# Optimization experiments

Hardware: AMD Instinct MI355X
Metric: run time of the kernel (lower is better)

Reference implementation:

```python
import jax, jax.numpy as jnp
import numpy as np

T, B, D_IN, HID, D_OUT = 512, 64, 1024, 512, 10


def _gru_dir(x, w_ih, w_hh, b_ih, b_hh, reverse):
    # x: [T,B,D]; w_ih: [3H,D]; w_hh: [3H,H]; biases: [3H]
    xp = jnp.einsum('tbd,gd->tbg', x, w_ih) + b_ih  # [T,B,3H]
    if reverse:
        xp = xp[::-1]
    H = w_hh.shape[1]

    def step(h, xt):
        gh = h @ w_hh.T + b_hh                      # [B,3H]
        xr, xz, xn = jnp.split(xt, 3, axis=-1)
        hr, hz, hn = jnp.split(gh, 3, axis=-1)
        r = jax.nn.sigmoid(xr + hr)
        z = jax.nn.sigmoid(xz + hz)
        n = jnp.tanh(xn + r * hn)
        h_new = (1.0 - z) * n + z * h
        return h_new, h_new

    h0 = jnp.zeros((x.shape[1], H), x.dtype)
    _, hs = jax.lax.scan(step, h0, xp)              # [T,B,H]
    if reverse:
        hs = hs[::-1]
    return hs


def setup_inputs() -> dict:
    key = jax.random.key(0)
    ks = jax.random.split(key, 20)
    k = 1.0 / np.sqrt(HID)
    u = lambda kk, sh, lim: jax.random.uniform(kk, sh, jnp.float32, -lim, lim)
    inp = {
        'numerical': jax.random.normal(ks[0], (B, 8), jnp.float32),
        'embedding': jax.random.normal(ks[1], (T, B, D_IN), jnp.float32),
        # GRU forward direction
        'w_ih_f': u(ks[2], (3 * HID, D_IN), k),
        'w_hh_f': u(ks[3], (3 * HID, HID), k),
        'b_ih_f': u(ks[4], (3 * HID,), k),
        'b_hh_f': u(ks[5], (3 * HID,), k),
        # GRU backward direction
        'w_ih_b': u(ks[6], (3 * HID, D_IN), k),
        'w_hh_b': u(ks[7], (3 * HID, HID), k),
        'b_ih_b': u(ks[8], (3 * HID,), k),
        'b_hh_b': u(ks[9], (3 * HID,), k),
        # attention params (normal std 0.05 per _create_weights)
        'attn_w': 0.05 * jax.random.normal(ks[10], (2 * HID, 2 * HID), jnp.float32),
        'attn_b': 0.05 * jax.random.normal(ks[11], (1, 2 * HID), jnp.float32),
        'ctx_w': 0.05 * jax.random.normal(ks[12], (2 * HID, 1), jnp.float32),
        # classifier: Linear(D_in -> hidden) -> ReLU -> Linear(hidden -> D_out)
        'cls_w1': u(ks[13], (D_IN, HID), 1.0 / np.sqrt(D_IN)),
        'cls_b1': u(ks[14], (HID,), 1.0 / np.sqrt(D_IN)),
        'cls_w2': u(ks[15], (HID, D_OUT), 1.0 / np.sqrt(HID)),
        'cls_b2': u(ks[16], (D_OUT,), 1.0 / np.sqrt(HID)),
    }
    return inp


def reference(numerical, embedding,
              w_ih_f, w_hh_f, b_ih_f, b_hh_f,
              w_ih_b, w_hh_b, b_ih_b, b_hh_b,
              attn_w, attn_b, ctx_w,
              cls_w1, cls_b1, cls_w2, cls_b2):
    # bidirectional GRU: [T,B,2H]
    hf = _gru_dir(embedding, w_ih_f, w_hh_f, b_ih_f, b_hh_f, reverse=False)
    hb = _gru_dir(embedding, w_ih_b, w_hh_b, b_ih_b, b_hh_b, reverse=True)
    f_output = jnp.concatenate([hf, hb], axis=-1)
    # additive attention: tanh(f W + b), then tanh(. @ ctx) -> scores [T,B]
    att = jnp.tanh(jnp.einsum('tbd,de->tbe', f_output, attn_w) + attn_b)
    scores = jnp.tanh(att @ ctx_w)[..., 0]          # [T,B]
    w = jax.nn.softmax(scores.T, axis=1)            # [B,T]
    ctx = jnp.einsum('tbd,bt->bd', f_output, w)     # [B,2H]
    # classifier
    hid = jax.nn.relu(ctx @ cls_w1 + cls_b1)
    out = hid @ cls_w2 + cls_b2                     # [B,D_OUT]
    return out
```

## Files before the change

### kernel.cpp

```cpp
#include <hip/hip_runtime.h>
#include <stdint.h>

#define T_   512
#define B_   64
#define DIN  1024
#define HID  512
#define G3   1536
#define NC   3072
#define MROWS 32768

typedef __bf16 bf16;
typedef __bf16 bf16x8 __attribute__((ext_vector_type(8)));
typedef float  f32x4  __attribute__((ext_vector_type(4)));

#define GLOBAL_AS __attribute__((address_space(1)))
#define LDS_AS    __attribute__((address_space(3)))

__device__ __forceinline__ uint16_t f2bf_bits(float x){
  union{float f; uint32_t u;} v; v.f = x;
  uint32_t u = v.u;
  u += 0x7FFFu + ((u >> 16) & 1u);
  return (uint16_t)(u >> 16);
}
__device__ __forceinline__ float bf2f_bits(uint16_t h){
  union{uint32_t u; float f;} v; v.u = ((uint32_t)h) << 16;
  return v.f;
}
__device__ __forceinline__ float sig_f(float x){
  return 1.f/(1.f + __expf(-x));
}
__device__ __forceinline__ float tanh_f(float x){
  return 1.f - 2.f/(1.f + __expf(2.f*x));
}

__global__ void k_conv_emb(const float* __restrict__ src, uint16_t* __restrict__ dst, long n8){
  long i = (long)blockIdx.x*blockDim.x + threadIdx.x;
  if(i >= n8) return;
  const float4* s = (const float4*)src;
  float4 a = s[i*2], b = s[i*2+1];
  uint32_t p0 = (uint32_t)f2bf_bits(a.x) | ((uint32_t)f2bf_bits(a.y) << 16);
  uint32_t p1 = (uint32_t)f2bf_bits(a.z) | ((uint32_t)f2bf_bits(a.w) << 16);
  uint32_t p2 = (uint32_t)f2bf_bits(b.x) | ((uint32_t)f2bf_bits(b.y) << 16);
  uint32_t p3 = (uint32_t)f2bf_bits(b.z) | ((uint32_t)f2bf_bits(b.w) << 16);
  ((uint4*)dst)[i] = make_uint4(p0,p1,p2,p3);
}

__global__ void k_conv_wcat(const float* __restrict__ wf, const float* __restrict__ wb, uint16_t* __restrict__ dst, int n){
  int i = blockIdx.x*256 + threadIdx.x;
  if(i >= n) return;
  float v = (i < G3*DIN) ? wf[i] : wb[i - G3*DIN];
  dst[i] = f2bf_bits(v);
}

__global__ void k_conv_awt(const float* __restrict__ aw, uint16_t* __restrict__ dst, int n){
  int i = blockIdx.x*256 + threadIdx.x;
  if(i >= n) return;
  int e = i >> 10, d = i & 1023;
  dst[i] = f2bf_bits(aw[d*1024 + e]);
}

__global__ void k_conv_whh(const float* __restrict__ wf, const float* __restrict__ wb, uint4* __restrict__ wmem){
  int idx = blockIdx.x*256 + threadIdx.x;
  if(idx >= 2*16*96*64) return;
  int c  = idx & 63;
  int t2 = idx >> 6;
  int lc = t2 % 96;
  int t3 = t2 / 96;
  int member = t3 & 15, dir = t3 >> 4;
  int ct = lc >> 4, rr = lc & 15;
  int gcol = (ct >> 1)*512 + member*32 + (ct & 1)*16 + rr;
  int csrc = c ^ (lc & 7);
  const float* src = (dir ? wb : wf) + (size_t)gcol*512 + csrc*8;
  float4 f0 = *(const float4*)src;
  float4 f1 = *(const float4*)(src + 4);
  uint32_t p0 = (uint32_t)f2bf_bits(f0.x) | ((uint32_t)f2bf_bits(f0.y) << 16);
  uint32_t p1 = (uint32_t)f2bf_bits(f0.z) | ((uint32_t)f2bf_bits(f0.w) << 16);
  uint32_t p2 = (uint32_t)f2bf_bits(f1.x) | ((uint32_t)f2bf_bits(f1.y) << 16);
  uint32_t p3 = (uint32_t)f2bf_bits(f1.z) | ((uint32_t)f2bf_bits(f1.w) << 16);
  wmem[idx] = make_uint4(p0,p1,p2,p3);
}

__launch_bounds__(256)
__global__ void k_gemm_xp(const uint16_t* __restrict__ A, const uint16_t* __restrict__ Bw,
                          const float* __restrict__ bihf, const float* __restrict__ bihb,
                          uint16_t* __restrict__ C)
{
  __shared__ uint16_t lA[2][128*32];
  __shared__ uint16_t lB[2][128*32];
  const int K = 1024;
  int bn = blockIdx.x, bm = blockIdx.y;
  int tid = threadIdx.x;
  int lane = tid & 63, wid = tid >> 6;
  int wm = wid >> 1, wn = wid & 1;
  int rowBase = bm*128, colBase = bn*128;
  int rg = lane >> 4, rr = lane & 15;

  auto stage = [&](int buf, int kt){
    #pragma unroll
    for(int i=0;i<2;i++){
      int e = (i*256 + tid)*8;
      int r = e >> 5, c = e & 31;
      __builtin_amdgcn_global_load_lds((const GLOBAL_AS void*)(A + (size_t)(rowBase + r)*K + kt*32 + c),
                                       (LDS_AS void*)&lA[buf][e], 16, 0, 0);
    }
    #pragma unroll
    for(int i=0;i<2;i++){
      int e = (i*256 + tid)*8;
      int r = e >> 5, c = e & 31;
      __builtin_amdgcn_global_load_lds((const GLOBAL_AS void*)(Bw + (size_t)(colBase + r)*K + kt*32 + c),
                                       (LDS_AS void*)&lB[buf][e], 16, 0, 0);
    }
  };

  f32x4 acc[4][4];
  #pragma unroll
  for(int mi=0;mi<4;mi++)
    #pragma unroll
    for(int ni=0;ni<4;ni++) acc[mi][ni] = (f32x4){0.f,0.f,0.f,0.f};

  stage(0, 0);
  __syncthreads();
  for(int kt=0; kt<32; kt++){
    int buf = kt & 1;
    if(kt+1 < 32) stage(buf^1, kt+1);
    bf16x8 af[4], bfv[4];
    #pragma unroll
    for(int mi=0;mi<4;mi++)
      af[mi] = *(const bf16x8*)&lA[buf][(wm*64 + mi*16 + rr)*32 + rg*8];
    #pragma unroll
    for(int ni=0;ni<4;ni++)
      bfv[ni] = *(const bf16x8*)&lB[buf][(wn*64 + ni*16 + rr)*32 + rg*8];
    #pragma unroll
    for(int mi=0;mi<4;mi++)
      #pragma unroll
      for(int ni=0;ni<4;ni++)
        acc[mi][ni] = __builtin_amdgcn_mfma_f32_16x16x32_bf16(af[mi], bfv[ni], acc[mi][ni], 0,0,0);
    __syncthreads();
  }

  #pragma unroll
  for(int ni=0;ni<4;ni++){
    int col = colBase + wn*64 + ni*16 + rr;
    float bv = (col < G3) ? bihf[col] : bihb[col - G3];
    int dircol = (col >= G3) ? 1 : 0;
    int cm = col - dircol*G3;
    int g  = cm >> 9;
    int j  = cm & 511;
    int mem = j >> 5, cc = j & 31;
    #pragma unroll
    for(int mi=0;mi<4;mi++){
      int row0 = rowBase + wm*64 + mi*16 + rg*4;
      int tt = row0 >> 6;
      int b0 = row0 & 63;
      int bgx = b0 >> 4, rr0 = b0 & 15;
      size_t ob = (((((size_t)dircol*512 + tt)*4 + bgx)*16 + mem)*3 + g)*512 + rr0*32 + cc;
      C[ob]      = f2bf_bits(acc[mi][ni][0]+bv);
      C[ob+32]   = f2bf_bits(acc[mi][ni][1]+bv);
      C[ob+64]   = f2bf_bits(acc[mi][ni][2]+bv);
      C[ob+96]   = f2bf_bits(acc[mi][ni][3]+bv);
    }
  }
}

__launch_bounds__(256)
__global__ void k_gemm_att(const uint16_t* __restrict__ A, const uint16_t* __restrict__ Bw,
                           const float* __restrict__ attn_b, const float* __restrict__ ctx_w,
                           float* __restrict__ scores_raw)
{
  __shared__ uint16_t lA[2][128*32];
  __shared__ uint16_t lB[2][128*32];
  const int K = 1024;
  int bn = blockIdx.x, bm = blockIdx.y;
  int tid = threadIdx.x;
  int lane = tid & 63, wid = tid >> 6;
  int wm = wid >> 1, wn = wid & 1;
  int rowBase = bm*128, colBase = bn*128;
  int rg = lane >> 4, rr = lane & 15;

  auto stage = [&](int buf, int kt){
    #pragma unroll
    for(int i=0;i<2;i++){
      int e = (i*256 + tid)*8;
      int r = e >> 5, c = e & 31;
      __builtin_amdgcn_global_load_lds((const GLOBAL_AS void*)(A + (size_t)(rowBase + r)*K + kt*32 + c),
                                       (LDS_AS void*)&lA[buf][e], 16, 0, 0);
    }
    #pragma unroll
    for(int i=0;i<2;i++){
      int e = (i*256 + tid)*8;
      int r = e >> 5, c = e & 31;
      __builtin_amdgcn_global_load_lds((const GLOBAL_AS void*)(Bw + (size_t)(colBase + r)*K + kt*32 + c),
                                       (LDS_AS void*)&lB[buf][e], 16, 0, 0);
    }
  };

  f32x4 acc[4][4];
  #pragma unroll
  for(int mi=0;mi<4;mi++)
    #pragma unroll
    for(int ni=0;ni<4;ni++) acc[mi][ni] = (f32x4){0.f,0.f,0.f,0.f};

  stage(0, 0);
  __syncthreads();
  for(int kt=0; kt<32; kt++){
    int buf = kt & 1;
    if(kt+1 < 32) stage(buf^1, kt+1);
    bf16x8 af[4], bfv[4];
    #pragma unroll
    for(int mi=0;mi<4;mi++)
      af[mi] = *(const bf16x8*)&lA[buf][(wm*64 + mi*16 + rr)*32 + rg*8];
    #pragma unroll
    for(int ni=0;ni<4;ni++)
      bfv[ni] = *(const bf16x8*)&lB[buf][(wn*64 + ni*16 + rr)*32 + rg*8];
    #pragma unroll
    for(int mi=0;mi<4;mi++)
      #pragma unroll
      for(int ni=0;ni<4;ni++)
        acc[mi][ni] = __builtin_amdgcn_mfma_f32_16x16x32_bf16(af[mi], bfv[ni], acc[mi][ni], 0,0,0);
    __syncthreads();
  }

  float ab[4], cw[4];
  #pragma unroll
  for(int ni=0;ni<4;ni++){
    int col = colBase + wn*64 + ni*16 + rr;
    ab[ni] = attn_b[col];
    cw[ni] = ctx_w[col];
  }
  #pragma unroll
  for(int mi=0;mi<4;mi++){
    #pragma unroll
    for(int r=0;r<4;r++){
      float part = 0.f;
      #pragma unroll
      for(int ni=0;ni<4;ni++) part += tanhf(acc[mi][ni][r] + ab[ni]) * cw[ni];
      #pragma unroll
      for(int off=1; off<16; off<<=1) part += __shfl_xor(part, off);
      if(rr == 0){
        int row = rowBase + wm*64 + mi*16 + rg*4 + r;
        atomicAdd(&scores_raw[row], part);
      }
    }
  }
}

__launch_bounds__(768, 3)
__global__ void k_recur(const uint16_t* __restrict__ xp,
                        const uint4* __restrict__ wmem,
                        const float* __restrict__ bhhf, const float* __restrict__ bhhb,
                        unsigned long long* __restrict__ tagbuf,
                        uint16_t* __restrict__ f_out)
{
  __shared__ uint16_t Wl[96*512];
  __shared__ uint16_t hl[16*512];
  __shared__ float    ghl[2*6*16*17];

  int bid = blockIdx.x;
  int dir = bid & 1, bg = (bid >> 1) & 3, member = bid >> 3;
  int jb = member*32;
  int tid = threadIdx.x;
  int lane = tid & 63, w = tid >> 6;
  int rr = lane & 15, rg = lane >> 4;
  int ct = w >> 1, kh = w & 1;

  const uint4* wsrc = wmem + (size_t)(dir*16 + member)*6144;
  for(int e = tid; e < 6144; e += 768)
    __builtin_amdgcn_global_load_lds((const GLOBAL_AS void*)(wsrc + e),
                                     (LDS_AS void*)&Wl[e*8], 16, 0, 0);
  for(int i = tid; i < 2*6*16*17; i += 768) ghl[i] = 0.f;

  int gcol = tid & 31;
  const float* bhh = dir ? bhhb : bhhf;
  float bR = 0.f, bZ = 0.f, bN = 0.f, hprev = 0.f;
  if(tid < 512){
    bR = bhh[jb + gcol];
    bZ = bhh[512 + jb + gcol];
    bN = bhh[1024 + jb + gcol];
  }

  int srow = tid >> 5;
  int sbase = tid & 31;
  int cswz = ((sbase >> 2) ^ (srow & 7));
  int lpos0 = srow*512 + cswz*8 + (sbase & 3)*2;

  __syncthreads();

  #pragma unroll 1
  for(int t = 0; t < 512; t++){
    int trow = dir ? (511 - t) : t;

    uint16_t xr16 = 0, xz16 = 0, xn16 = 0;
    if(tid < 512){
      const uint16_t* xb = xp + (((((size_t)dir*512 + trow)*4 + bg)*16 + member)*3)*512;
      xr16 = xb[tid];
      xz16 = xb[512 + tid];
      xn16 = xb[1024 + tid];
    }

    if(t > 0 && tid < 512){
      const unsigned long long* tb =
        tagbuf + ((size_t)((dir*2 + ((t-1) & 1))*4 + bg)*16 + srow)*256 + sbase;
      unsigned want = (unsigned)t;
      unsigned long long v0,v1,v2,v3,v4,v5,v6,v7;
      v0 = __hip_atomic_load(tb +   0, __ATOMIC_RELAXED, __HIP_MEMORY_SCOPE_AGENT);
      v1 = __hip_atomic_load(tb +  32, __ATOMIC_RELAXED, __HIP_MEMORY_SCOPE_AGENT);
      v2 = __hip_atomic_load(tb +  64, __ATOMIC_RELAXED, __HIP_MEMORY_SCOPE_AGENT);
      v3 = __hip_atomic_load(tb +  96, __ATOMIC_RELAXED, __HIP_MEMORY_SCOPE_AGENT);
      v4 = __hip_atomic_load(tb + 128, __ATOMIC_RELAXED, __HIP_MEMORY_SCOPE_AGENT);
      v5 = __hip_atomic_load(tb + 160, __ATOMIC_RELAXED, __HIP_MEMORY_SCOPE_AGENT);
      v6 = __hip_atomic_load(tb + 192, __ATOMIC_RELAXED, __HIP_MEMORY_SCOPE_AGENT);
      v7 = __hip_atomic_load(tb + 224, __ATOMIC_RELAXED, __HIP_MEMORY_SCOPE_AGENT);
      bool o0 = ((unsigned)v0 == want), o1 = ((unsigned)v1 == want);
      bool o2 = ((unsigned)v2 == want), o3 = ((unsigned)v3 == want);
      bool o4 = ((unsigned)v4 == want), o5 = ((unsigned)v5 == want);
      bool o6 = ((unsigned)v6 == want), o7 = ((unsigned)v7 == want);
      while(!(o0 & o1 & o2 & o3 & o4 & o5 & o6 & o7)){
        if(!o0){ v0 = __hip_atomic_load(tb +   0, __ATOMIC_RELAXED, __HIP_MEMORY_SCOPE_AGENT); o0 = ((unsigned)v0 == want); }
        if(!o1){ v1 = __hip_atomic_load(tb +  32, __ATOMIC_RELAXED, __HIP_MEMORY_SCOPE_AGENT); o1 = ((unsigned)v1 == want); }
        if(!o2){ v2 = __hip_atomic_load(tb +  64, __ATOMIC_RELAXED, __HIP_MEMORY_SCOPE_AGENT); o2 = ((unsigned)v2 == want); }
        if(!o3){ v3 = __hip_atomic_load(tb +  96, __ATOMIC_RELAXED, __HIP_MEMORY_SCOPE_AGENT); o3 = ((unsigned)v3 == want); }
        if(!o4){ v4 = __hip_atomic_load(tb + 128, __ATOMIC_RELAXED, __HIP_MEMORY_SCOPE_AGENT); o4 = ((unsigned)v4 == want); }
        if(!o5){ v5 = __hip_atomic_load(tb + 160, __ATOMIC_RELAXED, __HIP_MEMORY_SCOPE_AGENT); o5 = ((unsigned)v5 == want); }
        if(!o6){ v6 = __hip_atomic_load(tb + 192, __ATOMIC_RELAXED, __HIP_MEMORY_SCOPE_AGENT); o6 = ((unsigned)v6 == want); }
        if(!o7){ v7 = __hip_atomic_load(tb + 224, __ATOMIC_RELAXED, __HIP_MEMORY_SCOPE_AGENT); o7 = ((unsigned)v7 == want); }
      }
      *(uint32_t*)&hl[lpos0 +   0] = (uint32_t)(v0 >> 32);
      *(uint32_t*)&hl[lpos0 +  64] = (uint32_t)(v1 >> 32);
      *(uint32_t*)&hl[lpos0 + 128] = (uint32_t)(v2 >> 32);
      *(uint32_t*)&hl[lpos0 + 192] = (uint32_t)(v3 >> 32);
      *(uint32_t*)&hl[lpos0 + 256] = (uint32_t)(v4 >> 32);
      *(uint32_t*)&hl[lpos0 + 320] = (uint32_t)(v5 >> 32);
      *(uint32_t*)&hl[lpos0 + 384] = (uint32_t)(v6 >> 32);
      *(uint32_t*)&hl[lpos0 + 448] = (uint32_t)(v7 >> 32);
    }
    __syncthreads();

    if(t > 0){
      f32x4 acc = (f32x4){0.f,0.f,0.f,0.f};
      #pragma unroll
      for(int ks = 0; ks < 8; ks++){
        int ch = kh*32 + ks*4 + rg;
        int sw = (ch ^ (rr & 7))*8;
        bf16x8 a = *(const bf16x8*)&hl[rr*512 + sw];
        bf16x8 b = *(const bf16x8*)&Wl[(ct*16 + rr)*512 + sw];
        acc = __builtin_amdgcn_mfma_f32_16x16x32_bf16(a, b, acc, 0,0,0);
      }
      #pragma unroll
      for(int j = 0; j < 4; j++)
        ghl[((kh*6 + ct)*16 + rg*4 + j)*17 + rr] = acc[j];
    }
    __syncthreads();

    if(tid < 512){
      int grow = tid >> 5;
      int c16 = gcol >> 4, cc = gcol & 15;
      float gR = ghl[((0 + c16)*16 + grow)*17 + cc] + ghl[((6  + c16)*16 + grow)*17 + cc] + bR;
      float gZ = ghl[((2 + c16)*16 + grow)*17 + cc] + ghl[((8  + c16)*16 + grow)*17 + cc] + bZ;
      float gN = ghl[((4 + c16)*16 + grow)*17 + cc] + ghl[((10 + c16)*16 + grow)*17 + cc] + bN;
      float rv = sig_f(bf2f_bits(xr16) + gR);
      float zv = sig_f(bf2f_bits(xz16) + gZ);
      float nv = tanh_f(bf2f_bits(xn16) + rv*gN);
      float hnew = (1.f - zv)*nv + zv*hprev;
      hprev = hnew;
      unsigned hb = (unsigned)f2bf_bits(hnew);
      unsigned nb = (unsigned)__shfl_down((int)hb, 1);
      if((tid & 1) == 0){
        unsigned pk = hb | (nb << 16);
        int slot = member*16 + (gcol >> 1);
        unsigned long long pv = ((unsigned long long)pk << 32) | (unsigned)(t + 1);
        __hip_atomic_store(
          tagbuf + ((size_t)((dir*2 + (t & 1))*4 + bg)*16 + grow)*256 + slot,
          pv, __ATOMIC_RELAXED, __HIP_MEMORY_SCOPE_AGENT);
        *(unsigned*)&f_out[((size_t)trow*64 + bg*16 + grow)*1024 + dir*512 + jb + gcol] = pk;
      }
    }
  }
}

__global__ void k_softmax(const float* __restrict__ scores_raw, float* __restrict__ wsm){
  __shared__ float sv[512];
  __shared__ float red[8];
  int b = blockIdx.x;
  int tid = threadIdx.x;
  float mymax = -1e30f;
  for(int t = tid; t < 512; t += 256){
    float s = tanhf(scores_raw[t*64 + b]);
    sv[t] = s;
    mymax = fmaxf(mymax, s);
  }
  #pragma unroll
  for(int off=1; off<64; off<<=1) mymax = fmaxf(mymax, __shfl_xor(mymax, off));
  if((tid&63)==0) red[tid>>6] = mymax;
  __syncthreads();
  float bmax = fmaxf(fmaxf(red[0],red[1]), fmaxf(red[2],red[3]));
  __syncthreads();
  float mysum = 0.f;
  for(int t = tid; t < 512; t += 256){
    float e = __expf(sv[t] - bmax);
    sv[t] = e;
    mysum += e;
  }
  #pragma unroll
  for(int off=1; off<64; off<<=1) mysum += __shfl_xor(mysum, off);
  if((tid&63)==0) red[tid>>6] = mysum;
  __syncthreads();
  float inv = 1.f/(red[0]+red[1]+red[2]+red[3]);
  for(int t = tid; t < 512; t += 256) wsm[b*512 + t] = sv[t]*inv;
}

__global__ void k_ctx(const uint16_t* __restrict__ f_out, const float* __restrict__ wsm, float* __restrict__ ctx){
  __shared__ float wloc[512];
  int b = blockIdx.x >> 2, chunk = blockIdx.x & 3;
  int tid = threadIdx.x;
  for(int t = tid; t < 512; t += 256) wloc[t] = wsm[b*512 + t];
  __syncthreads();
  int d = chunk*256 + tid;
  float acc = 0.f;
  #pragma unroll 8
  for(int t = 0; t < 512; t++)
    acc += wloc[t] * bf2f_bits(f_out[(size_t)(t*64 + b)*1024 + d]);
  ctx[b*1024 + d] = acc;
}

__global__ void k_cls1(const float* __restrict__ ctx, const float* __restrict__ w1,
                       const float* __restrict__ b1, float* __restrict__ hid){
  int idx = blockIdx.x*256 + threadIdx.x;
  int b = idx >> 9, h = idx & 511;
  float acc = b1[h];
  for(int d = 0; d < 1024; d++) acc += ctx[b*1024 + d] * w1[d*512 + h];
  hid[idx] = fmaxf(acc, 0.f);
}

__global__ void k_cls2(const float* __restrict__ hid, const float* __restrict__ w2,
                       const float* __restrict__ b2, float* __restrict__ out){
  int idx = threadIdx.x;
  if(idx >= 640) return;
  int b = idx / 10, o = idx % 10;
  float acc = b2[o];
  for(int h = 0; h < 512; h++) acc += hid[b*512 + h] * w2[h*10 + o];
  out[idx] = acc;
}

extern "C" void kernel_launch(void* const* d_in, const int* in_sizes, int n_in,
                              void* d_out, int out_size, void* d_ws, size_t ws_size,
                              hipStream_t stream)
{
  const float* emb    = (const float*)d_in[1];
  const float* w_ih_f = (const float*)d_in[2];
  const float* w_hh_f = (const float*)d_in[3];
  const float* b_ih_f = (const float*)d_in[4];
  const float* b_hh_f = (const float*)d_in[5];
  const float* w_ih_b = (const float*)d_in[6];
  const float* w_hh_b = (const float*)d_in[7];
  const float* b_ih_b = (const float*)d_in[8];
  const float* b_hh_b = (const float*)d_in[9];
  const float* attn_w = (const float*)d_in[10];
  const float* attn_b = (const float*)d_in[11];
  const float* ctx_w  = (const float*)d_in[12];
  const float* cls_w1 = (const float*)d_in[13];
  const float* cls_b1 = (const float*)d_in[14];
  const float* cls_w2 = (const float*)d_in[15];
  const float* cls_b2 = (const float*)d_in[16];
  float* out = (float*)d_out;

  char* ws = (char*)d_ws;
  size_t off = 0;
  auto alloc = [&](size_t bytes){ void* p = ws + off; off += (bytes + 255) & ~(size_t)255; return p; };
  uint16_t* femb = (uint16_t*)alloc((size_t)MROWS*DIN*2);
  uint16_t* wcat = (uint16_t*)alloc((size_t)NC*DIN*2);
  uint16_t* xp   = (uint16_t*)alloc((size_t)MROWS*NC*2);
  uint16_t* awT  = (uint16_t*)alloc((size_t)1024*1024*2);
  uint4*    wmem = (uint4*)alloc((size_t)2*16*96*64*16);
  unsigned long long* tagbuf = (unsigned long long*)alloc((size_t)2*2*4*16*256*8);
  float* scraw   = (float*)alloc((size_t)MROWS*4);
  float* wsm     = (float*)alloc((size_t)B_*T_*4);
  float* ctx     = (float*)alloc((size_t)B_*1024*4);
  float* hid     = (float*)alloc((size_t)B_*512*4);

  hipMemsetAsync(tagbuf, 0, (size_t)2*2*4*16*256*8, stream);
  hipMemsetAsync(scraw, 0, (size_t)MROWS*4, stream);

  k_conv_emb<<<16384, 256, 0, stream>>>(emb, femb, (long)MROWS*DIN/8);
  k_conv_wcat<<<12288, 256, 0, stream>>>(w_ih_f, w_ih_b, wcat, NC*DIN);
  k_conv_awt<<<4096, 256, 0, stream>>>(attn_w, awT, 1024*1024);
  k_conv_whh<<<768, 256, 0, stream>>>(w_hh_f, w_hh_b, wmem);

  k_gemm_xp<<<dim3(24,256), 256, 0, stream>>>(femb, wcat, b_ih_f, b_ih_b, xp);

  k_recur<<<128, 768, 0, stream>>>(xp, wmem, b_hh_f, b_hh_b, tagbuf, femb );

  k_gemm_att<<<dim3(8,256), 256, 0, stream>>>(femb, awT, attn_b, ctx_w, scraw);
  k_softmax<<<64, 256, 0, stream>>>(scraw, wsm);
  k_ctx<<<256, 256, 0, stream>>>(femb, wsm, ctx);
  k_cls1<<<128, 256, 0, stream>>>(ctx, cls_w1, cls_b1, hid);
  k_cls2<<<1, 640, 0, stream>>>(hid, cls_w2, cls_b2, out);
}
```

Measured before the change: 1.720 ms.

## Interleave forward and backward GRU directions per block with register-resident weights

The recurrent kernel now runs both directions in one block (64 blocks instead of 128) and alternates forward and backward half-steps. Each direction's tag polling and x-projection loads are issued early, so one direction's cross-block wait overlaps the other's compute. Recurrent weights move from LDS into VGPRs held by empty asm constraints, which frees the LDS tile and removes the per-step LDS weight reads. In exchange, per-block serial work doubles and register pressure rises under the 768-thread launch bound, which may force spills.

Result: slower. 2.430 ms (+41.3%).

```diff
diff --git a/kernel.cpp b/kernel.cpp
--- a/kernel.cpp
+++ b/kernel.cpp
@@ -16,6 +16,8 @@
 #define GLOBAL_AS __attribute__((address_space(1)))
 #define LDS_AS    __attribute__((address_space(3)))
 
+#define LDT(p) __hip_atomic_load((p), __ATOMIC_RELAXED, __HIP_MEMORY_SCOPE_AGENT)
+
 __device__ __forceinline__ uint16_t f2bf_bits(float x){
   union{float f; uint32_t u;} v; v.f = x;
   uint32_t u = v.u;
@@ -31,6 +33,9 @@
 }
 __device__ __forceinline__ float tanh_f(float x){
   return 1.f - 2.f/(1.f + __expf(2.f*x));
+}
+__device__ __forceinline__ bf16x8 as_bf16x8(uint4 u){
+  union{uint4 a; bf16x8 b;} c; c.a = u; return c.b;
 }
 
 __global__ void k_conv_emb(const float* __restrict__ src, uint16_t* __restrict__ dst, long n8){
@@ -251,117 +256,144 @@
                         unsigned long long* __restrict__ tagbuf,
                         uint16_t* __restrict__ f_out)
 {
-  __shared__ uint16_t Wl[96*512];
   __shared__ uint16_t hl[16*512];
   __shared__ float    ghl[2*6*16*17];
 
   int bid = blockIdx.x;
-  int dir = bid & 1, bg = (bid >> 1) & 3, member = bid >> 3;
+  int bg = bid & 3, member = bid >> 2;
   int jb = member*32;
   int tid = threadIdx.x;
   int lane = tid & 63, w = tid >> 6;
   int rr = lane & 15, rg = lane >> 4;
   int ct = w >> 1, kh = w & 1;
-
-  const uint4* wsrc = wmem + (size_t)(dir*16 + member)*6144;
-  for(int e = tid; e < 6144; e += 768)
-    __builtin_amdgcn_global_load_lds((const GLOBAL_AS void*)(wsrc + e),
-                                     (LDS_AS void*)&Wl[e*8], 16, 0, 0);
+  int xm = rr & 7;
+
+  const uint4* wsl0 = wmem + (size_t)member*6144 + (ct*16 + rr)*64;
+  const uint4* wsl1 = wmem + (size_t)(16 + member)*6144 + (ct*16 + rr)*64;
+  uint4 wa0 = wsl0[(kh*32 +  0 + rg) ^ xm];
+  uint4 wa1 = wsl0[(kh*32 +  4 + rg) ^ xm];
+  uint4 wa2 = wsl0[(kh*32 +  8 + rg) ^ xm];
+  uint4 wa3 = wsl0[(kh*32 + 12 + rg) ^ xm];
+  uint4 wa4 = wsl0[(kh*32 + 16 + rg) ^ xm];
+  uint4 wa5 = wsl0[(kh*32 + 20 + rg) ^ xm];
+  uint4 wa6 = wsl0[(kh*32 + 24 + rg) ^ xm];
+  uint4 wa7 = wsl0[(kh*32 + 28 + rg) ^ xm];
+  uint4 wb0 = wsl1[(kh*32 +  0 + rg) ^ xm];
+  uint4 wb1 = wsl1[(kh*32 +  4 + rg) ^ xm];
+  uint4 wb2 = wsl1[(kh*32 +  8 + rg) ^ xm];
+  uint4 wb3 = wsl1[(kh*32 + 12 + rg) ^ xm];
+  uint4 wb4 = wsl1[(kh*32 + 16 + rg) ^ xm];
+  uint4 wb5 = wsl1[(kh*32 + 20 + rg) ^ xm];
+  uint4 wb6 = wsl1[(kh*32 + 24 + rg) ^ xm];
+  uint4 wb7 = wsl1[(kh*32 + 28 + rg) ^ xm];
+  asm volatile("" :: "v"(wa0.x), "v"(wa0.y), "v"(wa0.z), "v"(wa0.w),
+                     "v"(wa1.x), "v"(wa1.y), "v"(wa1.z), "v"(wa1.w));
+  asm volatile("" :: "v"(wa2.x), "v"(wa2.y), "v"(wa2.z), "v"(wa2.w),
+                     "v"(wa3.x), "v"(wa3.y), "v"(wa3.z), "v"(wa3.w));
+  asm volatile("" :: "v"(wa4.x), "v"(wa4.y), "v"(wa4.z), "v"(wa4.w),
+                     "v"(wa5.x), "v"(wa5.y), "v"(wa5.z), "v"(wa5.w));
+  asm volatile("" :: "v"(wa6.x), "v"(wa6.y), "v"(wa6.z), "v"(wa6.w),
+                     "v"(wa7.x), "v"(wa7.y), "v"(wa7.z), "v"(wa7.w));
+  asm volatile("" :: "v"(wb0.x), "v"(wb0.y), "v"(wb0.z), "v"(wb0.w),
+                     "v"(wb1.x), "v"(wb1.y), "v"(wb1.z), "v"(wb1.w));
+  asm volatile("" :: "v"(wb2.x), "v"(wb2.y), "v"(wb2.z), "v"(wb2.w),
+                     "v"(wb3.x), "v"(wb3.y), "v"(wb3.z), "v"(wb3.w));
+  asm volatile("" :: "v"(wb4.x), "v"(wb4.y), "v"(wb4.z), "v"(wb4.w),
+                     "v"(wb5.x), "v"(wb5.y), "v"(wb5.z), "v"(wb5.w));
+  asm volatile("" :: "v"(wb6.x), "v"(wb6.y), "v"(wb6.z), "v"(wb6.w),
+                     "v"(wb7.x), "v"(wb7.y), "v"(wb7.z), "v"(wb7.w));
+
   for(int i = tid; i < 2*6*16*17; i += 768) ghl[i] = 0.f;
 
   int gcol = tid & 31;
-  const float* bhh = dir ? bhhb : bhhf;
-  float bR = 0.f, bZ = 0.f, bN = 0.f, hprev = 0.f;
+  float bR0=0,bZ0=0,bN0=0,bR1=0,bZ1=0,bN1=0, hA=0.f, hB=0.f;
   if(tid < 512){
-    bR = bhh[jb + gcol];
-    bZ = bhh[512 + jb + gcol];
-    bN = bhh[1024 + jb + gcol];
-  }
-
-  int srow = tid >> 5;
-  int sbase = tid & 31;
-  int cswz = ((sbase >> 2) ^ (srow & 7));
+    bR0 = bhhf[jb + gcol]; bZ0 = bhhf[512 + jb + gcol]; bN0 = bhhf[1024 + jb + gcol];
+    bR1 = bhhb[jb + gcol]; bZ1 = bhhb[512 + jb + gcol]; bN1 = bhhb[1024 + jb + gcol];
+  }
+
+  int srow = tid >> 5, sbase = tid & 31;
+  int cswz = (sbase >> 2) ^ (srow & 7);
   int lpos0 = srow*512 + cswz*8 + (sbase & 3)*2;
 
+  unsigned long long pA0=0,pA1=0,pA2=0,pA3=0,pA4=0,pA5=0,pA6=0,pA7=0;
+  unsigned long long pB0=0,pB1=0,pB2=0,pB3=0,pB4=0,pB5=0,pB6=0,pB7=0;
+  uint16_t xAr=0,xAz=0,xAn=0, xBr=0,xBz=0,xBn=0;
+
+  if(tid < 512){
+    const uint16_t* xb = xp + (((size_t)bg*16 + member)*3)*512;
+    xAr = xb[tid]; xAz = xb[512 + tid]; xAn = xb[1024 + tid];
+  }
   __syncthreads();
 
   #pragma unroll 1
   for(int t = 0; t < 512; t++){
-    int trow = dir ? (511 - t) : t;
-
-    uint16_t xr16 = 0, xz16 = 0, xn16 = 0;
-    if(tid < 512){
-      const uint16_t* xb = xp + (((((size_t)dir*512 + trow)*4 + bg)*16 + member)*3)*512;
-      xr16 = xb[tid];
-      xz16 = xb[512 + tid];
-      xn16 = xb[1024 + tid];
-    }
-
     if(t > 0 && tid < 512){
       const unsigned long long* tb =
-        tagbuf + ((size_t)((dir*2 + ((t-1) & 1))*4 + bg)*16 + srow)*256 + sbase;
+        tagbuf + ((size_t)(((t-1)&1)*4 + bg)*16 + srow)*256 + sbase;
       unsigned want = (unsigned)t;
-      unsigned long long v0,v1,v2,v3,v4,v5,v6,v7;
-      v0 = __hip_atomic_load(tb +   0, __ATOMIC_RELAXED, __HIP_MEMORY_SCOPE_AGENT);
-      v1 = __hip_atomic_load(tb +  32, __ATOMIC_RELAXED, __HIP_MEMORY_SCOPE_AGENT);
-      v2 = __hip_atomic_load(tb +  64, __ATOMIC_RELAXED, __HIP_MEMORY_SCOPE_AGENT);
-      v3 = __hip_atomic_load(tb +  96, __ATOMIC_RELAXED, __HIP_MEMORY_SCOPE_AGENT);
-      v4 = __hip_atomic_load(tb + 128, __ATOMIC_RELAXED, __HIP_MEMORY_SCOPE_AGENT);
-      v5 = __hip_atomic_load(tb + 160, __ATOMIC_RELAXED, __HIP_MEMORY_SCOPE_AGENT);
-      v6 = __hip_atomic_load(tb + 192, __ATOMIC_RELAXED, __HIP_MEMORY_SCOPE_AGENT);
-      v7 = __hip_atomic_load(tb + 224, __ATOMIC_RELAXED, __HIP_MEMORY_SCOPE_AGENT);
-      bool o0 = ((unsigned)v0 == want), o1 = ((unsigned)v1 == want);
-      bool o2 = ((unsigned)v2 == want), o3 = ((unsigned)v3 == want);
-      bool o4 = ((unsigned)v4 == want), o5 = ((unsigned)v5 == want);
-      bool o6 = ((unsigned)v6 == want), o7 = ((unsigned)v7 == want);
-      while(!(o0 & o1 & o2 & o3 & o4 & o5 & o6 & o7)){
-        if(!o0){ v0 = __hip_atomic_load(tb +   0, __ATOMIC_RELAXED, __HIP_MEMORY_SCOPE_AGENT); o0 = ((unsigned)v0 == want); }
-        if(!o1){ v1 = __hip_atomic_load(tb +  32, __ATOMIC_RELAXED, __HIP_MEMORY_SCOPE_AGENT); o1 = ((unsigned)v1 == want); }
-        if(!o2){ v2 = __hip_atomic_load(tb +  64, __ATOMIC_RELAXED, __HIP_MEMORY_SCOPE_AGENT); o2 = ((unsigned)v2 == want); }
-        if(!o3){ v3 = __hip_atomic_load(tb +  96, __ATOMIC_RELAXED, __HIP_MEMORY_SCOPE_AGENT); o3 = ((unsigned)v3 == want); }
-        if(!o4){ v4 = __hip_atomic_load(tb + 128, __ATOMIC_RELAXED, __HIP_MEMORY_SCOPE_AGENT); o4 = ((unsigned)v4 == want); }
-        if(!o5){ v5 = __hip_atomic_load(tb + 160, __ATOMIC_RELAXED, __HIP_MEMORY_SCOPE_AGENT); o5 = ((unsigned)v5 == want); }
-        if(!o6){ v6 = __hip_atomic_load(tb + 192, __ATOMIC_RELAXED, __HIP_MEMORY_SCOPE_AGENT); o6 = ((unsigned)v6 == want); }
-        if(!o7){ v7 = __hip_atomic_load(tb + 224, __ATOMIC_RELAXED, __HIP_MEMORY_SCOPE_AGENT); o7 = ((unsigned)v7 == want); }
+      bool ok = ((unsigned)pA0==want)&((unsigned)pA1==want)&((unsigned)pA2==want)&((unsigned)pA3==want)
+              & ((unsigned)pA4==want)&((unsigned)pA5==want)&((unsigned)pA6==want)&((unsigned)pA7==want);
+      while(!ok){
+        pA0 = LDT(tb+0);   pA1 = LDT(tb+32);  pA2 = LDT(tb+64);  pA3 = LDT(tb+96);
+        pA4 = LDT(tb+128); pA5 = LDT(tb+160); pA6 = LDT(tb+192); pA7 = LDT(tb+224);
+        ok = ((unsigned)pA0==want)&((unsigned)pA1==want)&((unsigned)pA2==want)&((unsigned)pA3==want)
+           & ((unsigned)pA4==want)&((unsigned)pA5==want)&((unsigned)pA6==want)&((unsigned)pA7==want);
       }
-      *(uint32_t*)&hl[lpos0 +   0] = (uint32_t)(v0 >> 32);
-      *(uint32_t*)&hl[lpos0 +  64] = (uint32_t)(v1 >> 32);
-      *(uint32_t*)&hl[lpos0 + 128] = (uint32_t)(v2 >> 32);
-      *(uint32_t*)&hl[lpos0 + 192] = (uint32_t)(v3 >> 32);
-      *(uint32_t*)&hl[lpos0 + 256] = (uint32_t)(v4 >> 32);
-      *(uint32_t*)&hl[lpos0 + 320] = (uint32_t)(v5 >> 32);
-      *(uint32_t*)&hl[lpos0 + 384] = (uint32_t)(v6 >> 32);
-      *(uint32_t*)&hl[lpos0 + 448] = (uint32_t)(v7 >> 32);
+      *(uint32_t*)&hl[lpos0 +   0] = (uint32_t)(pA0 >> 32);
+      *(uint32_t*)&hl[lpos0 +  64] = (uint32_t)(pA1 >> 32);
+      *(uint32_t*)&hl[lpos0 + 128] = (uint32_t)(pA2 >> 32);
+      *(uint32_t*)&hl[lpos0 + 192] = (uint32_t)(pA3 >> 32);
+      *(uint32_t*)&hl[lpos0 + 256] = (uint32_t)(pA4 >> 32);
+      *(uint32_t*)&hl[lpos0 + 320] = (uint32_t)(pA5 >> 32);
+      *(uint32_t*)&hl[lpos0 + 384] = (uint32_t)(pA6 >> 32);
+      *(uint32_t*)&hl[lpos0 + 448] = (uint32_t)(pA7 >> 32);
+    }
+    if(tid < 512){
+      if(t > 0){
+        const unsigned long long* tb =
+          tagbuf + ((size_t)((2 + ((t-1)&1))*4 + bg)*16 + srow)*256 + sbase;
+        pB0 = LDT(tb+0);   pB1 = LDT(tb+32);  pB2 = LDT(tb+64);  pB3 = LDT(tb+96);
+        pB4 = LDT(tb+128); pB5 = LDT(tb+160); pB6 = LDT(tb+192); pB7 = LDT(tb+224);
+      }
+      const uint16_t* xb = xp + (((((size_t)512 + (511 - t))*4 + bg)*16 + member)*3)*512;
+      xBr = xb[tid]; xBz = xb[512 + tid]; xBn = xb[1024 + tid];
     }
     __syncthreads();
-
     if(t > 0){
       f32x4 acc = (f32x4){0.f,0.f,0.f,0.f};
-      #pragma unroll
-      for(int ks = 0; ks < 8; ks++){
-        int ch = kh*32 + ks*4 + rg;
-        int sw = (ch ^ (rr & 7))*8;
-        bf16x8 a = *(const bf16x8*)&hl[rr*512 + sw];
-        bf16x8 b = *(const bf16x8*)&Wl[(ct*16 + rr)*512 + sw];
-        acc = __builtin_amdgcn_mfma_f32_16x16x32_bf16(a, b, acc, 0,0,0);
-      }
+      bf16x8 a0 = *(const bf16x8*)&hl[rr*512 + ((kh*32 +  0 + rg) ^ xm)*8];
+      acc = __builtin_amdgcn_mfma_f32_16x16x32_bf16(a0, as_bf16x8(wa0), acc, 0,0,0);
+      bf16x8 a1 = *(const bf16x8*)&hl[rr*512 + ((kh*32 +  4 + rg) ^ xm)*8];
+      acc = __builtin_amdgcn_mfma_f32_16x16x32_bf16(a1, as_bf16x8(wa1), acc, 0,0,0);
+      bf16x8 a2 = *(const bf16x8*)&hl[rr*512 + ((kh*32 +  8 + rg) ^ xm)*8];
+      acc = __builtin_amdgcn_mfma_f32_16x16x32_bf16(a2, as_bf16x8(wa2), acc, 0,0,0);
+      bf16x8 a3 = *(const bf16x8*)&hl[rr*512 + ((kh*32 + 12 + rg) ^ xm)*8];
+      acc = __builtin_amdgcn_mfma_f32_16x16x32_bf16(a3, as_bf16x8(wa3), acc, 0,0,0);
+      bf16x8 a4 = *(const bf16x8*)&hl[rr*512 + ((kh*32 + 16 + rg) ^ xm)*8];
+      acc = __builtin_amdgcn_mfma_f32_16x16x32_bf16(a4, as_bf16x8(wa4), acc, 0,0,0);
+      bf16x8 a5 = *(const bf16x8*)&hl[rr*512 + ((kh*32 + 20 + rg) ^ xm)*8];
+      acc = __builtin_amdgcn_mfma_f32_16x16x32_bf16(a5, as_bf16x8(wa5), acc, 0,0,0);
+      bf16x8 a6 = *(const bf16x8*)&hl[rr*512 + ((kh*32 + 24 + rg) ^ xm)*8];
+      acc = __builtin_amdgcn_mfma_f32_16x16x32_bf16(a6, as_bf16x8(wa6), acc, 0,0,0);
+      bf16x8 a7 = *(const bf16x8*)&hl[rr*512 + ((kh*32 + 28 + rg) ^ xm)*8];
+      acc = __builtin_amdgcn_mfma_f32_16x16x32_bf16(a7, as_bf16x8(wa7), acc, 0,0,0);
       #pragma unroll
       for(int j = 0; j < 4; j++)
         ghl[((kh*6 + ct)*16 + rg*4 + j)*17 + rr] = acc[j];
     }
     __syncthreads();
-
     if(tid < 512){
       int grow = tid >> 5;
       int c16 = gcol >> 4, cc = gcol & 15;
-      float gR = ghl[((0 + c16)*16 + grow)*17 + cc] + ghl[((6  + c16)*16 + grow)*17 + cc] + bR;
-      float gZ = ghl[((2 + c16)*16 + grow)*17 + cc] + ghl[((8  + c16)*16 + grow)*17 + cc] + bZ;
-      float gN = ghl[((4 + c16)*16 + grow)*17 + cc] + ghl[((10 + c16)*16 + grow)*17 + cc] + bN;
-      float rv = sig_f(bf2f_bits(xr16) + gR);
-      float zv = sig_f(bf2f_bits(xz16) + gZ);
-      float nv = tanh_f(bf2f_bits(xn16) + rv*gN);
-      float hnew = (1.f - zv)*nv + zv*hprev;
-      hprev = hnew;
+      float gR = ghl[((0 + c16)*16 + grow)*17 + cc] + ghl[((6  + c16)*16 + grow)*17 + cc] + bR0;
+      float gZ = ghl[((2 + c16)*16 + grow)*17 + cc] + ghl[((8  + c16)*16 + grow)*17 + cc] + bZ0;
+      float gN = ghl[((4 + c16)*16 + grow)*17 + cc] + ghl[((10 + c16)*16 + grow)*17 + cc] + bN0;
+      float rv = sig_f(bf2f_bits(xAr) + gR);
+      float zv = sig_f(bf2f_bits(xAz) + gZ);
+      float nv = tanh_f(bf2f_bits(xAn) + rv*gN);
+      float hnew = (1.f - zv)*nv + zv*hA;
+      hA = hnew;
       unsigned hb = (unsigned)f2bf_bits(hnew);
       unsigned nb = (unsigned)__shfl_down((int)hb, 1);
       if((tid & 1) == 0){
@@ -369,9 +401,86 @@
         int slot = member*16 + (gcol >> 1);
         unsigned long long pv = ((unsigned long long)pk << 32) | (unsigned)(t + 1);
         __hip_atomic_store(
-          tagbuf + ((size_t)((dir*2 + (t & 1))*4 + bg)*16 + grow)*256 + slot,
+          tagbuf + ((size_t)((t&1)*4 + bg)*16 + grow)*256 + slot,
           pv, __ATOMIC_RELAXED, __HIP_MEMORY_SCOPE_AGENT);
-        *(unsigned*)&f_out[((size_t)trow*64 + bg*16 + grow)*1024 + dir*512 + jb + gcol] = pk;
+        *(unsigned*)&f_out[((size_t)t*64 + bg*16 + grow)*1024 + jb + gcol] = pk;
+      }
+    }
+
+    if(t > 0 && tid < 512){
+      const unsigned long long* tb =
+        tagbuf + ((size_t)((2 + ((t-1)&1))*4 + bg)*16 + srow)*256 + sbase;
+      unsigned want = (unsigned)t;
+      bool ok = ((unsigned)pB0==want)&((unsigned)pB1==want)&((unsigned)pB2==want)&((unsigned)pB3==want)
+              & ((unsigned)pB4==want)&((unsigned)pB5==want)&((unsigned)pB6==want)&((unsigned)pB7==want);
+      while(!ok){
+        pB0 = LDT(tb+0);   pB1 = LDT(tb+32);  pB2 = LDT(tb+64);  pB3 = LDT(tb+96);
+        pB4 = LDT(tb+128); pB5 = LDT(tb+160); pB6 = LDT(tb+192); pB7 = LDT(tb+224);
+        ok = ((unsigned)pB0==want)&((unsigned)pB1==want)&((unsigned)pB2==want)&((unsigned)pB3==want)
+           & ((unsigned)pB4==want)&((unsigned)pB5==want)&((unsigned)pB6==want)&((unsigned)pB7==want);
+      }
+      *(uint32_t*)&hl[lpos0 +   0] = (uint32_t)(pB0 >> 32);
+      *(uint32_t*)&hl[lpos0 +  64] = (uint32_t)(pB1 >> 32);
+      *(uint32_t*)&hl[lpos0 + 128] = (uint32_t)(pB2 >> 32);
+      *(uint32_t*)&hl[lpos0 + 192] = (uint32_t)(pB3 >> 32);
+      *(uint32_t*)&hl[lpos0 + 256] = (uint32_t)(pB4 >> 32);
+      *(uint32_t*)&hl[lpos0 + 320] = (uint32_t)(pB5 >> 32);
+      *(uint32_t*)&hl[lpos0 + 384] = (uint32_t)(pB6 >> 32);
+      *(uint32_t*)&hl[lpos0 + 448] = (uint32_t)(pB7 >> 32);
+    }
+    if(tid < 512){
+      const unsigned long long* tb =
+        tagbuf + ((size_t)((t&1)*4 + bg)*16 + srow)*256 + sbase;
+      pA0 = LDT(tb+0);   pA1 = LDT(tb+32);  pA2 = LDT(tb+64);  pA3 = LDT(tb+96);
+      pA4 = LDT(tb+128); pA5 = LDT(tb+160); pA6 = LDT(tb+192); pA7 = LDT(tb+224);
+      const uint16_t* xb = xp + (((((size_t)(t + 1))*4 + bg)*16 + member)*3)*512;
+      xAr = xb[tid]; xAz = xb[512 + tid]; xAn = xb[1024 + tid];
+    }
+    __syncthreads();
+    if(t > 0){
+      f32x4 acc = (f32x4){0.f,0.f,0.f,0.f};
+      bf16x8 a0 = *(const bf16x8*)&hl[rr*512 + ((kh*32 +  0 + rg) ^ xm)*8];
+      acc = __builtin_amdgcn_mfma_f32_16x16x32_bf16(a0, as_bf16x8(wb0), acc, 0,0,0);
+      bf16x8 a1 = *(const bf16x8*)&hl[rr*512 + ((kh*32 +  4 + rg) ^ xm)*8];
+      acc = __builtin_amdgcn_mfma_f32_16x16x32_bf16(a1, as_bf16x8(wb1), acc, 0,0,0);
+      bf16x8 a2 = *(const bf16x8*)&hl[rr*512 + ((kh*32 +  8 + rg) ^ xm)*8];
+      acc = __builtin_amdgcn_mfma_f32_16x16x32_bf16(a2, as_bf16x8(wb2), acc, 0,0,0);
+      bf16x8 a3 = *(const bf16x8*)&hl[rr*512 + ((kh*32 + 12 + rg) ^ xm)*8];
+      acc = __builtin_amdgcn_mfma_f32_16x16x32_bf16(a3, as_bf16x8(wb3), acc, 0,0,0);
+      bf16x8 a4 = *(const bf16x8*)&hl[rr*512 + ((kh*32 + 16 + rg) ^ xm)*8];
+      acc = __builtin_amdgcn_mfma_f32_16x16x32_bf16(a4, as_bf16x8(wb4), acc, 0,0,0);
+      bf16x8 a5 = *(const bf16x8*)&hl[rr*512 + ((kh*32 + 20 + rg) ^ xm)*8];
+      acc = __builtin_amdgcn_mfma_f32_16x16x32_bf16(a5, as_bf16x8(wb5), acc, 0,0,0);
+      bf16x8 a6 = *(const bf16x8*)&hl[rr*512 + ((kh*32 + 24 + rg) ^ xm)*8];
+      acc = __builtin_amdgcn_mfma_f32_16x16x32_bf16(a6, as_bf16x8(wb6), acc, 0,0,0);
+      bf16x8 a7 = *(const bf16x8*)&hl[rr*512 + ((kh*32 + 28 + rg) ^ xm)*8];
+      acc = __builtin_amdgcn_mfma_f32_16x16x32_bf16(a7, as_bf16x8(wb7), acc, 0,0,0);
+      #pragma unroll
+      for(int j = 0; j < 4; j++)
+        ghl[((kh*6 + ct)*16 + rg*4 + j)*17 + rr] = acc[j];
+    }
+    __syncthreads();
+    if(tid < 512){
+      int grow = tid >> 5;
+      int c16 = gcol >> 4, cc = gcol & 15;
+      float gR = ghl[((0 + c16)*16 + grow)*17 + cc] + ghl[((6  + c16)*16 + grow)*17 + cc] + bR1;
+      float gZ = ghl[((2 + c16)*16 + grow)*17 + cc] + ghl[((8  + c16)*16 + grow)*17 + cc] + bZ1;
+      float gN = ghl[((4 + c16)*16 + grow)*17 + cc] + ghl[((10 + c16)*16 + grow)*17 + cc] + bN1;
+      float rv = sig_f(bf2f_bits(xBr) + gR);
+      float zv = sig_f(bf2f_bits(xBz) + gZ);
+      float nv = tanh_f(bf2f_bits(xBn) + rv*gN);
+      float hnew = (1.f - zv)*nv + zv*hB;
+      hB = hnew;
+      unsigned hb = (unsigned)f2bf_bits(hnew);
+      unsigned nb = (unsigned)__shfl_down((int)hb, 1);
+      if((tid & 1) == 0){
+        unsigned pk = hb | (nb << 16);
+        int slot = member*16 + (gcol >> 1);
+        unsigned long long pv = ((unsigned long long)pk << 32) | (unsigned)(t + 1);
+        __hip_atomic_store(
+          tagbuf + ((size_t)((2 + (t&1))*4 + bg)*16 + grow)*256 + slot,
+          pv, __ATOMIC_RELAXED, __HIP_MEMORY_SCOPE_AGENT);
+        *(unsigned*)&f_out[((size_t)(511 - t)*64 + bg*16 + grow)*1024 + 512 + jb + gcol] = pk;
       }
     }
   }
@@ -477,8 +586,8 @@
   float* ctx     = (float*)alloc((size_t)B_*1024*4);
   float* hid     = (float*)alloc((size_t)B_*512*4);
 
-  hipMemsetAsync(tagbuf, 0, (size_t)2*2*4*16*256*8, stream);
-  hipMemsetAsync(scraw, 0, (size_t)MROWS*4, stream);
+  (void)hipMemsetAsync(tagbuf, 0, (size_t)2*2*4*16*256*8, stream);
+  (void)hipMemsetAsync(scraw, 0, (size_t)MROWS*4, stream);
 
   k_conv_emb<<<16384, 256, 0, stream>>>(emb, femb, (long)MROWS*DIN/8);
   k_conv_wcat<<<12288, 256, 0, stream>>>(w_ih_f, w_ih_b, wcat, NC*DIN);
@@ -487,7 +596,7 @@
 
   k_gemm_xp<<<dim3(24,256), 256, 0, stream>>>(femb, wcat, b_ih_f, b_ih_b, xp);
 
-  k_recur<<<128, 768, 0, stream>>>(xp, wmem, b_hh_f, b_hh_b, tagbuf, femb );
+  k_recur<<<64, 768, 0, stream>>>(xp, wmem, b_hh_f, b_hh_b, tagbuf, femb );
 
   k_gemm_att<<<dim3(8,256), 256, 0, stream>>>(femb, awT, attn_b, ctx_w, scraw);
   k_softmax<<<64, 256, 0, stream>>>(scraw, wsm);
```
